# Kernel optimization log

Hardware: AMD Instinct MI355X
Metric: run time of the kernel (lower is better)

Reference implementation:

```python
import jax, jax.numpy as jnp
import numpy as np

N, M, D_IN, D_OUT = 100000, 1024, 64, 64


def setup_inputs() -> dict:
    key = jax.random.key(0)
    ks = jax.random.split(key, 8)
    # kaiming_uniform_ bound for fan_in = D_IN: sqrt(6 / fan_in) with a=sqrt(5) default? torch's
    # kaiming_uniform_ default (a=0) gives bound = sqrt(6/fan_in); exact init is irrelevant for math.
    bound = float(np.sqrt(6.0 / D_IN))
    return {
        "x": jax.random.normal(ks[0], (N, D_IN), dtype=jnp.float32),
        "neighbors": jax.random.normal(ks[1], (M, D_IN), dtype=jnp.float32),
        "Wq": jax.random.uniform(ks[2], (D_OUT, D_IN), jnp.float32, -bound, bound),
        "bq": jnp.zeros((D_OUT,), jnp.float32),
        "Wk": jax.random.uniform(ks[3], (D_OUT, D_IN), jnp.float32, -bound, bound),
        "bk": jnp.zeros((D_OUT,), jnp.float32),
        "Wv": jax.random.uniform(ks[4], (D_OUT, D_IN), jnp.float32, -bound, bound),
        "bv": jnp.zeros((D_OUT,), jnp.float32),
    }


def reference(x, neighbors, Wq, bq, Wk, bk, Wv, bv):
    # q: [N, D_OUT], k: [M, D_OUT]
    q = x @ Wq.T + bq
    k = neighbors @ Wk.T + bk
    # scores: [N, M] -- same math as sum(q[:,None,:] * k[None,:,:], axis=2) but via GEMM
    scores = q @ k.T
    attn = jax.nn.softmax(scores, axis=1)
    # attn @ neighbors: [N, D_IN], then value projection -> [N, D_OUT]
    agg = attn @ neighbors
    return agg @ Wv.T + bv
```

## Files before the change

### kernel.cpp

```cpp
#include <hip/hip_runtime.h>


#define N_ROWS 100000
#define LOG2E 1.44269504088896f
#define GATE_THR 11.5424f

typedef __attribute__((ext_vector_type(8))) _Float16 half8;
typedef __attribute__((ext_vector_type(2))) __fp16   fp16x2;
typedef __attribute__((ext_vector_type(4))) float    f32x4;

#define MFMA16(a,b,c) __builtin_amdgcn_mfma_f32_16x16x32_f16((a),(b),(c),0,0,0)

static __device__ __forceinline__ f32x4 zero4() {
    f32x4 v = {0.f, 0.f, 0.f, 0.f};
    return v;
}

__global__ __launch_bounds__(256)
void prep_kernel(const float* __restrict__ nb, const float* __restrict__ Wq,
                 const float* __restrict__ bq, const float* __restrict__ Wk,
                 unsigned short* __restrict__ GFh, unsigned short* __restrict__ GFl,
                 float* __restrict__ uW, unsigned short* __restrict__ KF,
                 unsigned short* __restrict__ VF)
{
    __shared__ __align__(16) float sm[8192];
    const int tid = threadIdx.x;
    if (blockIdx.x == 0) {
        const float4* wk4 = (const float4*)Wk;
        const float4* wq4 = (const float4*)Wq;
        float4* dk = (float4*)sm;
        float4* dq = (float4*)(sm + 4096);
        #pragma unroll
        for (int u = 0; u < 4; u++) {
            dk[u * 256 + tid] = wk4[u * 256 + tid];
            dq[u * 256 + tid] = wq4[u * 256 + tid];
        }
        __syncthreads();
        const int e2 = tid & 63, e1g = (tid >> 6) * 16;
        float g[16];
        #pragma unroll
        for (int q = 0; q < 16; q++) g[q] = 0.f;
        for (int w = 0; w < 64; w++) {
            float kv = sm[w * 64 + e2];
            const float* wqp = sm + 4096 + w * 64 + e1g;
            #pragma unroll
            for (int q = 0; q < 16; q++) g[q] = fmaf(wqp[q], kv, g[q]);
        }
        union { half8 h; uint4 u; } ph0, pl0, ph1, pl1;
        #pragma unroll
        for (int i = 0; i < 8; i++) {
            _Float16 h0 = (_Float16)g[i];
            ph0.h[i] = h0; pl0.h[i] = (_Float16)(g[i] - (float)h0);
            _Float16 h1 = (_Float16)g[8 + i];
            ph1.h[i] = h1; pl1.h[i] = (_Float16)(g[8 + i] - (float)h1);
        }
        const int mt = e2 >> 4, cc = e2 & 15;
        const int ks = tid >> 7, Q0 = 2 * ((tid >> 6) & 1);
        const int f  = mt * 2 + ks;
        *(uint4*)(GFh + (f * 64 + Q0 * 16 + cc) * 8)       = ph0.u;
        *(uint4*)(GFh + (f * 64 + (Q0 + 1) * 16 + cc) * 8) = ph1.u;
        *(uint4*)(GFl + (f * 64 + Q0 * 16 + cc) * 8)       = pl0.u;
        *(uint4*)(GFl + (f * 64 + (Q0 + 1) * 16 + cc) * 8) = pl1.u;
        if (tid < 64) {
            float uu = 0.f;
            for (int w = 0; w < 64; w++) uu = fmaf(bq[w], sm[w * 64 + tid], uu);
            uW[tid] = uu;
        }
    } else {
        const int j0 = (blockIdx.x - 1) * 64;
        const int T0 = (blockIdx.x - 1) * 2;
        {
            const int jr = tid >> 2, c0 = (tid & 3) * 16;
            const float* np = nb + (size_t)(j0 + jr) * 64 + c0;
            #pragma unroll
            for (int u = 0; u < 4; u++) {
                float4 v = *(const float4*)(np + 4 * u);
                sm[jr * 65 + c0 + 4 * u]     = v.x;
                sm[jr * 65 + c0 + 4 * u + 1] = v.y;
                sm[jr * 65 + c0 + 4 * u + 2] = v.z;
                sm[jr * 65 + c0 + 4 * u + 3] = v.w;
            }
        }
        #pragma unroll
        for (int s = 0; s < 2; s++) {
            const int slot = tid + 256 * s;
            const int tt = (slot >> 8) & 1, f = (slot >> 6) & 3, ln = slot & 63;
            const int t = f >> 1, h = f & 1, Qw = ln >> 4, cw = ln & 15;
            const int key = ((cw >> 3) & 1) * 16 + ((cw >> 2) & 1) * 8 + 4 * t + (cw & 3);
            const float* kp = nb + (size_t)((T0 + tt) * 32 + key) * 64 + h * 32 + Qw * 8;
            float b[8];
            *(float4*)b       = *(const float4*)kp;
            *(float4*)(b + 4) = *(const float4*)(kp + 4);
            union { half8 hh; uint4 u; } pk;
            #pragma unroll
            for (int i = 0; i < 8; i++) pk.hh[i] = (_Float16)b[i];
            *(uint4*)(KF + (size_t)(T0 + tt) * 2048 + f * 512 + ln * 8) = pk.u;
        }
        __syncthreads();
        #pragma unroll
        for (int s = 0; s < 2; s++) {
            const int slot = tid + 256 * s;
            const int tt = (slot >> 8) & 1, dt = (slot >> 6) & 3, ln = slot & 63;
            const int Qw = ln >> 4, cw = ln & 15;
            union { half8 hh; uint4 u; } pv;
            #pragma unroll
            for (int i = 0; i < 8; i++)
                pv.hh[i] = (_Float16)sm[(tt * 32 + Qw * 8 + i) * 65 + dt * 16 + cw];
            *(uint4*)(VF + (size_t)(T0 + tt) * 2048 + dt * 512 + ln * 8) = pv.u;
        }
    }
}

static __device__ __forceinline__ void load4(half8 (&dst)[4], const unsigned short* base) {
    #pragma unroll
    for (int f = 0; f < 4; f++) dst[f] = *(const half8*)(base + f * 512);
}

static __device__ __forceinline__ void qk_tile(
    const half8 (&k)[4], const half8 (&qh)[2][2], const half8 (&ql)[2][2],
    f32x4 (&S)[2][2])
{
    #pragma unroll
    for (int t = 0; t < 2; t++)
        #pragma unroll
        for (int qt = 0; qt < 2; qt++) {
            f32x4 s = MFMA16(k[2 * t],     qh[qt][0], zero4());
            s = MFMA16(k[2 * t + 1], qh[qt][1], s);
            s = MFMA16(k[2 * t],     ql[qt][0], s);
            s = MFMA16(k[2 * t + 1], ql[qt][1], s);
            S[t][qt] = s;
        }
}

static __device__ __forceinline__ void sm_pv(
    const f32x4 (&S)[2][2], const half8 (&vA)[4],
    f32x4 (&acc)[2][4], float (&mrow)[2], float (&lrow)[2])
{
    float pmax[2];
    #pragma unroll
    for (int qt = 0; qt < 2; qt++) {
        pmax[qt] = fmaxf(fmaxf(fmaxf(S[0][qt][0], S[0][qt][1]),
                               fmaxf(S[0][qt][2], S[0][qt][3])),
                         fmaxf(fmaxf(S[1][qt][0], S[1][qt][1]),
                               fmaxf(S[1][qt][2], S[1][qt][3])));
    }
    if (__any((pmax[0] > mrow[0] + GATE_THR) | (pmax[1] > mrow[1] + GATE_THR))) {
        #pragma unroll
        for (int qt = 0; qt < 2; qt++) {
            float cm = pmax[qt];
            cm = fmaxf(cm, __shfl_xor(cm, 16));
            cm = fmaxf(cm, __shfl_xor(cm, 32));
            const float mn = fmaxf(mrow[qt], cm);
            const float sc = __builtin_amdgcn_exp2f(mrow[qt] - mn);
            mrow[qt] = mn;
            lrow[qt] *= sc;
            #pragma unroll
            for (int dt = 0; dt < 4; dt++)
                #pragma unroll
                for (int r = 0; r < 4; r++) acc[qt][dt][r] *= sc;
        }
    }
    union { half8 v; fp16x2 h2[4]; } pk[2];
    #pragma unroll
    for (int qt = 0; qt < 2; qt++) {
        const float mref = mrow[qt];
        float p[8]; float ps = 0.f;
        #pragma unroll
        for (int r = 0; r < 4; r++) {
            p[r]     = __builtin_amdgcn_exp2f(S[0][qt][r] - mref);
            p[4 + r] = __builtin_amdgcn_exp2f(S[1][qt][r] - mref);
        }
        #pragma unroll
        for (int i = 0; i < 8; i++) ps += p[i];
        lrow[qt] += ps;
        #pragma unroll
        for (int j = 0; j < 4; j++)
            pk[qt].h2[j] = __builtin_amdgcn_cvt_pkrtz(p[2 * j], p[2 * j + 1]);
    }
    #pragma unroll
    for (int dt = 0; dt < 4; dt++) {
        acc[0][dt] = MFMA16(vA[dt], pk[0].v, acc[0][dt]);
        acc[1][dt] = MFMA16(vA[dt], pk[1].v, acc[1][dt]);
    }
}

__global__ __launch_bounds__(64, 3)
void attn_kernel(const float* __restrict__ x,
                 const unsigned short* __restrict__ GFh,
                 const unsigned short* __restrict__ GFl,
                 const float* __restrict__ uW,
                 const unsigned short* __restrict__ KF,
                 const unsigned short* __restrict__ VF,
                 const float* __restrict__ Wv,
                 const float* __restrict__ bv,
                 float* __restrict__ out)
{
    __shared__ __align__(16) float slice[1088];
    const int lane = threadIdx.x & 63;
    const int Q    = lane >> 4;
    const int c    = lane & 15;
    const int rbase = blockIdx.x * 32;

    half8 qh[2][2], ql[2][2];
    #pragma unroll
    for (int rt = 0; rt < 2; rt++) {
        const int row = rbase + rt * 16 + c;
        half8 xh[2], xl[2];
        #pragma unroll
        for (int ks = 0; ks < 2; ks++) {
            const float* xp = x + (size_t)row * 64 + ks * 32 + Q * 8;
            float a[8];
            *(float4*)a       = *(const float4*)xp;
            *(float4*)(a + 4) = *(const float4*)(xp + 4);
            #pragma unroll
            for (int i = 0; i < 8; i++) {
                _Float16 h = (_Float16)a[i];
                xh[ks][i] = h;
                xl[ks][i] = (_Float16)(a[i] - (float)h);
            }
        }
        #pragma unroll
        for (int mt = 0; mt < 4; mt++) {
            f32x4 Cm = zero4();
            #pragma unroll
            for (int ks = 0; ks < 2; ks++) {
                half8 gh = *(const half8*)(GFh + ((mt * 2 + ks) * 64 + lane) * 8);
                half8 gl = *(const half8*)(GFl + ((mt * 2 + ks) * 64 + lane) * 8);
                Cm = MFMA16(gh, xh[ks], Cm);
                Cm = MFMA16(gh, xl[ks], Cm);
                Cm = MFMA16(gl, xh[ks], Cm);
            }
            *(f32x4*)(slice + c * 68 + mt * 16 + 4 * Q) = Cm;
        }
        __builtin_amdgcn_s_waitcnt(0);
        #pragma unroll
        for (int ks = 0; ks < 2; ks++) {
            const float* qp = slice + c * 68 + ks * 32 + Q * 8;
            const float* up = uW + ks * 32 + Q * 8;
            #pragma unroll
            for (int i = 0; i < 8; i++) {
                float val = (qp[i] + up[i]) * LOG2E;
                _Float16 h = (_Float16)val;
                qh[rt][ks][i] = h;
                ql[rt][ks][i] = (_Float16)(val - (float)h);
            }
        }
        __builtin_amdgcn_s_waitcnt(0);
    }

    f32x4 acc[2][4];
    #pragma unroll
    for (int qt = 0; qt < 2; qt++)
        #pragma unroll
        for (int dt = 0; dt < 4; dt++) acc[qt][dt] = zero4();
    float mrow[2] = { -3.0e38f, -3.0e38f };
    float lrow[2] = { 0.f, 0.f };

    const unsigned short* kfl = KF + lane * 8;
    const unsigned short* vfl = VF + lane * 8;
    half8 kA[4], vA[4];
    f32x4 Sa[2][2], Sb[2][2];

    load4(kA, kfl);
    load4(vA, vfl);
    qk_tile(kA, qh, ql, Sa);
    load4(kA, kfl + 2048);

    #pragma unroll 1
    for (int TT = 0; TT < 16; TT++) {
        qk_tile(kA, qh, ql, Sb);
        {   int Tn = 2 * TT + 2; if (Tn > 31) Tn = 31;
            load4(kA, kfl + (size_t)Tn * 2048); }
        sm_pv(Sa, vA, acc, mrow, lrow);
        {   int Tn = 2 * TT + 1; if (Tn > 31) Tn = 31;
            load4(vA, vfl + (size_t)Tn * 2048); }
        qk_tile(kA, qh, ql, Sa);
        {   int Tn = 2 * TT + 3; if (Tn > 31) Tn = 31;
            load4(kA, kfl + (size_t)Tn * 2048); }
        sm_pv(Sb, vA, acc, mrow, lrow);
        {   int Tn = 2 * TT + 2; if (Tn > 31) Tn = 31;
            load4(vA, vfl + (size_t)Tn * 2048); }
    }

    #pragma unroll
    for (int qt = 0; qt < 2; qt++) {
        float l = lrow[qt];
        l += __shfl_xor(l, 16);
        l += __shfl_xor(l, 32);
        const float rl = 1.f / l;
        #pragma unroll
        for (int dt = 0; dt < 4; dt++)
            #pragma unroll
            for (int r = 0; r < 4; r++) acc[qt][dt][r] *= rl;
    }
    half8 wf[4][2];
    #pragma unroll
    for (int mt = 0; mt < 4; mt++)
        #pragma unroll
        for (int ks = 0; ks < 2; ks++) {
            const float* wp = Wv + (size_t)(mt * 16 + c) * 64 + ks * 32 + Q * 8;
            #pragma unroll
            for (int i = 0; i < 8; i++) wf[mt][ks][i] = (_Float16)wp[i];
        }
    const int srcA = 32 * (Q & 1) + c;
    const int srcB = srcA + 16;
    const bool hi = (Q >> 1) & 1;
    f32x4 o[2][4];
    #pragma unroll
    for (int qt = 0; qt < 2; qt++) {
        half8 pe[2];
        #pragma unroll
        for (int ks = 0; ks < 2; ks++) {
            #pragma unroll
            for (int r = 0; r < 4; r++) {
                float a0 = __shfl(acc[qt][2 * ks + 0][r], srcA);
                float a1 = __shfl(acc[qt][2 * ks + 1][r], srcA);
                float b0 = __shfl(acc[qt][2 * ks + 0][r], srcB);
                float b1 = __shfl(acc[qt][2 * ks + 1][r], srcB);
                pe[ks][r]     = (_Float16)(hi ? a1 : a0);
                pe[ks][4 + r] = (_Float16)(hi ? b1 : b0);
            }
        }
        #pragma unroll
        for (int mt = 0; mt < 4; mt++) {
            f32x4 t = MFMA16(wf[mt][0], pe[0], zero4());
            o[qt][mt] = MFMA16(wf[mt][1], pe[1], t);
        }
    }
    #pragma unroll
    for (int qt = 0; qt < 2; qt++) {
        const int row = rbase + qt * 16 + c;
        #pragma unroll
        for (int mt = 0; mt < 4; mt++) {
            const float4 bf = *(const float4*)(bv + mt * 16 + 4 * Q);
            float4 vv = make_float4(o[qt][mt][0] + bf.x, o[qt][mt][1] + bf.y,
                                    o[qt][mt][2] + bf.z, o[qt][mt][3] + bf.w);
            *(float4*)(out + (size_t)row * 64 + mt * 16 + 4 * Q) = vv;
        }
    }
}

extern "C" void kernel_launch(void* const* d_in, const int* in_sizes, int n_in,
                              void* d_out, int out_size, void* d_ws, size_t ws_size,
                              hipStream_t stream)
{
    const float* x  = (const float*)d_in[0];
    const float* nb = (const float*)d_in[1];
    const float* Wq = (const float*)d_in[2];
    const float* bq = (const float*)d_in[3];
    const float* Wk = (const float*)d_in[4];
    const float* Wv = (const float*)d_in[6];
    const float* bv = (const float*)d_in[7];
    float* out = (float*)d_out;

    char* ws = (char*)d_ws;
    unsigned short* GFh = (unsigned short*)(ws);
    unsigned short* GFl = (unsigned short*)(ws + 8192);
    float*          uW  = (float*)(ws + 16384);
    unsigned short* KF  = (unsigned short*)(ws + 16640);
    unsigned short* VF  = (unsigned short*)(ws + 147712);

    prep_kernel<<<17, 256, 0, stream>>>(nb, Wq, bq, Wk, GFh, GFl, uW, KF, VF);
    const int grid = N_ROWS / 32;
    attn_kernel<<<grid, 64, 0, stream>>>(x, GFh, GFl, uW, KF, VF, Wv, bv, out);
}
```

Baseline: 152.4 us.

## Process 64 rows per wave to reuse K/V fragments across more query tiles

```diff
diff --git a/kernel.cpp b/kernel.cpp
--- a/kernel.cpp
+++ b/kernel.cpp
@@ -67,46 +67,40 @@
             uW[tid] = uu;
         }
     } else {
-        const int j0 = (blockIdx.x - 1) * 64;
-        const int T0 = (blockIdx.x - 1) * 2;
+        const int T0 = blockIdx.x - 1;
+        const int j0 = T0 * 32;
         {
-            const int jr = tid >> 2, c0 = (tid & 3) * 16;
+            const int jr = tid >> 3, c0 = (tid & 7) * 8;
             const float* np = nb + (size_t)(j0 + jr) * 64 + c0;
-            #pragma unroll
-            for (int u = 0; u < 4; u++) {
-                float4 v = *(const float4*)(np + 4 * u);
-                sm[jr * 65 + c0 + 4 * u]     = v.x;
-                sm[jr * 65 + c0 + 4 * u + 1] = v.y;
-                sm[jr * 65 + c0 + 4 * u + 2] = v.z;
-                sm[jr * 65 + c0 + 4 * u + 3] = v.w;
-            }
-        }
-        #pragma unroll
-        for (int s = 0; s < 2; s++) {
-            const int slot = tid + 256 * s;
-            const int tt = (slot >> 8) & 1, f = (slot >> 6) & 3, ln = slot & 63;
+            float4 v0 = *(const float4*)np;
+            float4 v1 = *(const float4*)(np + 4);
+            sm[jr * 65 + c0 + 0] = v0.x; sm[jr * 65 + c0 + 1] = v0.y;
+            sm[jr * 65 + c0 + 2] = v0.z; sm[jr * 65 + c0 + 3] = v0.w;
+            sm[jr * 65 + c0 + 4] = v1.x; sm[jr * 65 + c0 + 5] = v1.y;
+            sm[jr * 65 + c0 + 6] = v1.z; sm[jr * 65 + c0 + 7] = v1.w;
+        }
+        {
+            const int f = tid >> 6, ln = tid & 63;
             const int t = f >> 1, h = f & 1, Qw = ln >> 4, cw = ln & 15;
             const int key = ((cw >> 3) & 1) * 16 + ((cw >> 2) & 1) * 8 + 4 * t + (cw & 3);
-            const float* kp = nb + (size_t)((T0 + tt) * 32 + key) * 64 + h * 32 + Qw * 8;
+            const float* kp = nb + (size_t)(j0 + key) * 64 + h * 32 + Qw * 8;
             float b[8];
             *(float4*)b       = *(const float4*)kp;
             *(float4*)(b + 4) = *(const float4*)(kp + 4);
             union { half8 hh; uint4 u; } pk;
             #pragma unroll
             for (int i = 0; i < 8; i++) pk.hh[i] = (_Float16)b[i];
-            *(uint4*)(KF + (size_t)(T0 + tt) * 2048 + f * 512 + ln * 8) = pk.u;
+            *(uint4*)(KF + (size_t)T0 * 2048 + f * 512 + ln * 8) = pk.u;
         }
         __syncthreads();
-        #pragma unroll
-        for (int s = 0; s < 2; s++) {
-            const int slot = tid + 256 * s;
-            const int tt = (slot >> 8) & 1, dt = (slot >> 6) & 3, ln = slot & 63;
+        {
+            const int dt = tid >> 6, ln = tid & 63;
             const int Qw = ln >> 4, cw = ln & 15;
             union { half8 hh; uint4 u; } pv;
             #pragma unroll
             for (int i = 0; i < 8; i++)
-                pv.hh[i] = (_Float16)sm[(tt * 32 + Qw * 8 + i) * 65 + dt * 16 + cw];
-            *(uint4*)(VF + (size_t)(T0 + tt) * 2048 + dt * 512 + ln * 8) = pv.u;
+                pv.hh[i] = (_Float16)sm[(Qw * 8 + i) * 65 + dt * 16 + cw];
+            *(uint4*)(VF + (size_t)T0 * 2048 + dt * 512 + ln * 8) = pv.u;
         }
     }
 }
@@ -116,75 +110,7 @@
     for (int f = 0; f < 4; f++) dst[f] = *(const half8*)(base + f * 512);
 }
 
-static __device__ __forceinline__ void qk_tile(
-    const half8 (&k)[4], const half8 (&qh)[2][2], const half8 (&ql)[2][2],
-    f32x4 (&S)[2][2])
-{
-    #pragma unroll
-    for (int t = 0; t < 2; t++)
-        #pragma unroll
-        for (int qt = 0; qt < 2; qt++) {
-            f32x4 s = MFMA16(k[2 * t],     qh[qt][0], zero4());
-            s = MFMA16(k[2 * t + 1], qh[qt][1], s);
-            s = MFMA16(k[2 * t],     ql[qt][0], s);
-            s = MFMA16(k[2 * t + 1], ql[qt][1], s);
-            S[t][qt] = s;
-        }
-}
-
-static __device__ __forceinline__ void sm_pv(
-    const f32x4 (&S)[2][2], const half8 (&vA)[4],
-    f32x4 (&acc)[2][4], float (&mrow)[2], float (&lrow)[2])
-{
-    float pmax[2];
-    #pragma unroll
-    for (int qt = 0; qt < 2; qt++) {
-        pmax[qt] = fmaxf(fmaxf(fmaxf(S[0][qt][0], S[0][qt][1]),
-                               fmaxf(S[0][qt][2], S[0][qt][3])),
-                         fmaxf(fmaxf(S[1][qt][0], S[1][qt][1]),
-                               fmaxf(S[1][qt][2], S[1][qt][3])));
-    }
-    if (__any((pmax[0] > mrow[0] + GATE_THR) | (pmax[1] > mrow[1] + GATE_THR))) {
-        #pragma unroll
-        for (int qt = 0; qt < 2; qt++) {
-            float cm = pmax[qt];
-            cm = fmaxf(cm, __shfl_xor(cm, 16));
-            cm = fmaxf(cm, __shfl_xor(cm, 32));
-            const float mn = fmaxf(mrow[qt], cm);
-            const float sc = __builtin_amdgcn_exp2f(mrow[qt] - mn);
-            mrow[qt] = mn;
-            lrow[qt] *= sc;
-            #pragma unroll
-            for (int dt = 0; dt < 4; dt++)
-                #pragma unroll
-                for (int r = 0; r < 4; r++) acc[qt][dt][r] *= sc;
-        }
-    }
-    union { half8 v; fp16x2 h2[4]; } pk[2];
-    #pragma unroll
-    for (int qt = 0; qt < 2; qt++) {
-        const float mref = mrow[qt];
-        float p[8]; float ps = 0.f;
-        #pragma unroll
-        for (int r = 0; r < 4; r++) {
-            p[r]     = __builtin_amdgcn_exp2f(S[0][qt][r] - mref);
-            p[4 + r] = __builtin_amdgcn_exp2f(S[1][qt][r] - mref);
-        }
-        #pragma unroll
-        for (int i = 0; i < 8; i++) ps += p[i];
-        lrow[qt] += ps;
-        #pragma unroll
-        for (int j = 0; j < 4; j++)
-            pk[qt].h2[j] = __builtin_amdgcn_cvt_pkrtz(p[2 * j], p[2 * j + 1]);
-    }
-    #pragma unroll
-    for (int dt = 0; dt < 4; dt++) {
-        acc[0][dt] = MFMA16(vA[dt], pk[0].v, acc[0][dt]);
-        acc[1][dt] = MFMA16(vA[dt], pk[1].v, acc[1][dt]);
-    }
-}
-
-__global__ __launch_bounds__(64, 3)
+__global__ __launch_bounds__(64, 2)
 void attn_kernel(const float* __restrict__ x,
                  const unsigned short* __restrict__ GFh,
                  const unsigned short* __restrict__ GFl,
@@ -199,12 +125,13 @@
     const int lane = threadIdx.x & 63;
     const int Q    = lane >> 4;
     const int c    = lane & 15;
-    const int rbase = blockIdx.x * 32;
-
-    half8 qh[2][2], ql[2][2];
-    #pragma unroll
-    for (int rt = 0; rt < 2; rt++) {
-        const int row = rbase + rt * 16 + c;
+    const int rbase = blockIdx.x * 64;
+
+    half8 qh[4][2], ql[4][2];
+    #pragma unroll
+    for (int rt = 0; rt < 4; rt++) {
+        int row = rbase + rt * 16 + c;
+        if (row > N_ROWS - 1) row = N_ROWS - 1;
         half8 xh[2], xl[2];
         #pragma unroll
         for (int ks = 0; ks < 2; ks++) {
@@ -248,42 +175,103 @@
         __builtin_amdgcn_s_waitcnt(0);
     }
 
-    f32x4 acc[2][4];
-    #pragma unroll
-    for (int qt = 0; qt < 2; qt++)
+    f32x4 acc[4][4];
+    #pragma unroll
+    for (int qt = 0; qt < 4; qt++)
         #pragma unroll
         for (int dt = 0; dt < 4; dt++) acc[qt][dt] = zero4();
-    float mrow[2] = { -3.0e38f, -3.0e38f };
-    float lrow[2] = { 0.f, 0.f };
+    float mrow[4] = { -3.0e38f, -3.0e38f, -3.0e38f, -3.0e38f };
+    float lrow[4] = { 0.f, 0.f, 0.f, 0.f };
 
     const unsigned short* kfl = KF + lane * 8;
     const unsigned short* vfl = VF + lane * 8;
     half8 kA[4], vA[4];
-    f32x4 Sa[2][2], Sb[2][2];
-
     load4(kA, kfl);
     load4(vA, vfl);
-    qk_tile(kA, qh, ql, Sa);
-    load4(kA, kfl + 2048);
 
     #pragma unroll 1
-    for (int TT = 0; TT < 16; TT++) {
-        qk_tile(kA, qh, ql, Sb);
-        {   int Tn = 2 * TT + 2; if (Tn > 31) Tn = 31;
-            load4(kA, kfl + (size_t)Tn * 2048); }
-        sm_pv(Sa, vA, acc, mrow, lrow);
-        {   int Tn = 2 * TT + 1; if (Tn > 31) Tn = 31;
-            load4(vA, vfl + (size_t)Tn * 2048); }
-        qk_tile(kA, qh, ql, Sa);
-        {   int Tn = 2 * TT + 3; if (Tn > 31) Tn = 31;
-            load4(kA, kfl + (size_t)Tn * 2048); }
-        sm_pv(Sb, vA, acc, mrow, lrow);
-        {   int Tn = 2 * TT + 2; if (Tn > 31) Tn = 31;
-            load4(vA, vfl + (size_t)Tn * 2048); }
+    for (int TT = 0; TT < 32; TT++) {
+        const int Tn = (TT < 31) ? TT + 1 : 31;
+
+        f32x4 S[2][4];
+        #pragma unroll
+        for (int t = 0; t < 2; t++)
+            #pragma unroll
+            for (int qt = 0; qt < 4; qt++) {
+                f32x4 s = MFMA16(kA[2 * t],     qh[qt][0], zero4());
+                s = MFMA16(kA[2 * t + 1], qh[qt][1], s);
+                s = MFMA16(kA[2 * t],     ql[qt][0], s);
+                s = MFMA16(kA[2 * t + 1], ql[qt][1], s);
+                S[t][qt] = s;
+            }
+        load4(kA, kfl + (size_t)Tn * 2048);
+
+        float pmax[4];
+        #pragma unroll
+        for (int qt = 0; qt < 4; qt++) {
+            pmax[qt] = fmaxf(fmaxf(fmaxf(S[0][qt][0], S[0][qt][1]),
+                                   fmaxf(S[0][qt][2], S[0][qt][3])),
+                             fmaxf(fmaxf(S[1][qt][0], S[1][qt][1]),
+                                   fmaxf(S[1][qt][2], S[1][qt][3])));
+        }
+        const bool need = (pmax[0] > mrow[0] + GATE_THR) | (pmax[1] > mrow[1] + GATE_THR) |
+                          (pmax[2] > mrow[2] + GATE_THR) | (pmax[3] > mrow[3] + GATE_THR);
+        if (__any(need)) {
+            #pragma unroll
+            for (int qt = 0; qt < 4; qt++) {
+                float cm = pmax[qt];
+                cm = fmaxf(cm, __shfl_xor(cm, 16));
+                cm = fmaxf(cm, __shfl_xor(cm, 32));
+                const float mn = fmaxf(mrow[qt], cm);
+                const float sc = __builtin_amdgcn_exp2f(mrow[qt] - mn);
+                mrow[qt] = mn;
+                lrow[qt] *= sc;
+                #pragma unroll
+                for (int dt = 0; dt < 4; dt++)
+                    #pragma unroll
+                    for (int r = 0; r < 4; r++) acc[qt][dt][r] *= sc;
+            }
+        }
+
+        union { half8 v; fp16x2 h2[4]; } pB[4];
+        #pragma unroll
+        for (int qt = 0; qt < 4; qt++) {
+            const float mref = mrow[qt];
+            float p[8];
+            #pragma unroll
+            for (int r = 0; r < 4; r++) {
+                p[r]     = __builtin_amdgcn_exp2f(S[0][qt][r] - mref);
+                p[4 + r] = __builtin_amdgcn_exp2f(S[1][qt][r] - mref);
+            }
+            lrow[qt] += ((p[0] + p[1]) + (p[2] + p[3])) + ((p[4] + p[5]) + (p[6] + p[7]));
+            #pragma unroll
+            for (int j = 0; j < 4; j++)
+                pB[qt].h2[j] = __builtin_amdgcn_cvt_pkrtz(p[2 * j], p[2 * j + 1]);
+        }
+        #pragma unroll
+        for (int dt = 0; dt < 4; dt++) {
+            acc[0][dt] = MFMA16(vA[dt], pB[0].v, acc[0][dt]);
+            acc[1][dt] = MFMA16(vA[dt], pB[1].v, acc[1][dt]);
+            acc[2][dt] = MFMA16(vA[dt], pB[2].v, acc[2][dt]);
+            acc[3][dt] = MFMA16(vA[dt], pB[3].v, acc[3][dt]);
+        }
+        load4(vA, vfl + (size_t)Tn * 2048);
     }
 
-    #pragma unroll
-    for (int qt = 0; qt < 2; qt++) {
+    half8 wf[4][2];
+    #pragma unroll
+    for (int mt = 0; mt < 4; mt++)
+        #pragma unroll
+        for (int ks = 0; ks < 2; ks++) {
+            const float* wp = Wv + (size_t)(mt * 16 + c) * 64 + ks * 32 + Q * 8;
+            #pragma unroll
+            for (int i = 0; i < 8; i++) wf[mt][ks][i] = (_Float16)wp[i];
+        }
+    const int srcA = 32 * (Q & 1) + c;
+    const int srcB = srcA + 16;
+    const bool hi = (Q >> 1) & 1;
+    #pragma unroll
+    for (int qt = 0; qt < 4; qt++) {
         float l = lrow[qt];
         l += __shfl_xor(l, 16);
         l += __shfl_xor(l, 32);
@@ -292,22 +280,6 @@
         for (int dt = 0; dt < 4; dt++)
             #pragma unroll
             for (int r = 0; r < 4; r++) acc[qt][dt][r] *= rl;
-    }
-    half8 wf[4][2];
-    #pragma unroll
-    for (int mt = 0; mt < 4; mt++)
-        #pragma unroll
-        for (int ks = 0; ks < 2; ks++) {
-            const float* wp = Wv + (size_t)(mt * 16 + c) * 64 + ks * 32 + Q * 8;
-            #pragma unroll
-            for (int i = 0; i < 8; i++) wf[mt][ks][i] = (_Float16)wp[i];
-        }
-    const int srcA = 32 * (Q & 1) + c;
-    const int srcB = srcA + 16;
-    const bool hi = (Q >> 1) & 1;
-    f32x4 o[2][4];
-    #pragma unroll
-    for (int qt = 0; qt < 2; qt++) {
         half8 pe[2];
         #pragma unroll
         for (int ks = 0; ks < 2; ks++) {
@@ -321,21 +293,17 @@
                 pe[ks][4 + r] = (_Float16)(hi ? b1 : b0);
             }
         }
-        #pragma unroll
-        for (int mt = 0; mt < 4; mt++) {
-            f32x4 t = MFMA16(wf[mt][0], pe[0], zero4());
-            o[qt][mt] = MFMA16(wf[mt][1], pe[1], t);
-        }
-    }
-    #pragma unroll
-    for (int qt = 0; qt < 2; qt++) {
         const int row = rbase + qt * 16 + c;
-        #pragma unroll
-        for (int mt = 0; mt < 4; mt++) {
-            const float4 bf = *(const float4*)(bv + mt * 16 + 4 * Q);
-            float4 vv = make_float4(o[qt][mt][0] + bf.x, o[qt][mt][1] + bf.y,
-                                    o[qt][mt][2] + bf.z, o[qt][mt][3] + bf.w);
-            *(float4*)(out + (size_t)row * 64 + mt * 16 + 4 * Q) = vv;
+        if (row < N_ROWS) {
+            #pragma unroll
+            for (int mt = 0; mt < 4; mt++) {
+                f32x4 t = MFMA16(wf[mt][0], pe[0], zero4());
+                f32x4 o = MFMA16(wf[mt][1], pe[1], t);
+                const float4 bf = *(const float4*)(bv + mt * 16 + 4 * Q);
+                float4 vv = make_float4(o[0] + bf.x, o[1] + bf.y,
+                                        o[2] + bf.z, o[3] + bf.w);
+                *(float4*)(out + (size_t)row * 64 + mt * 16 + 4 * Q) = vv;
+            }
         }
     }
 }
@@ -360,7 +328,7 @@
     unsigned short* KF  = (unsigned short*)(ws + 16640);
     unsigned short* VF  = (unsigned short*)(ws + 147712);
 
-    prep_kernel<<<17, 256, 0, stream>>>(nb, Wq, bq, Wk, GFh, GFl, uW, KF, VF);
-    const int grid = N_ROWS / 32;
+    prep_kernel<<<33, 256, 0, stream>>>(nb, Wq, bq, Wk, GFh, GFl, uW, KF, VF);
+    const int grid = (N_ROWS + 63) / 64;
     attn_kernel<<<grid, 64, 0, stream>>>(x, GFh, GFl, uW, KF, VF, Wv, bv, out);
 }
```

New measurement: 151.2 us. About the same (-0.8%).
